# Kernel tuning notes

Hardware: AMD Instinct MI355X
Metric: run time of the kernel (lower is better)

The kernel has to match this reference:

```python
import jax, jax.numpy as jnp
import numpy as np

V, D, H, HD, T, FF, L = 32000, 1024, 16, 64, 1024, 4096, 8
B, S = 2, 1024
EPS = 1e-5


def setup_inputs() -> dict:
    key = jax.random.key(0)
    ks = jax.random.split(key, 14)
    s = 0.02
    return {
        "input_ids": jax.random.randint(ks[0], (B, S), 0, V),
        "emb": jax.random.normal(ks[1], (V, D), jnp.float32) * s,
        "Wu": jax.random.normal(ks[2], (L, 3 * T, D), jnp.float32) * s,
        "Wo": jax.random.normal(ks[3], (L, D, T), jnp.float32) * s,
        "n1w": jnp.ones((L, D), jnp.float32),
        "n1b": jnp.zeros((L, D), jnp.float32),
        "n2w": jnp.ones((L, D), jnp.float32),
        "n2b": jnp.zeros((L, D), jnp.float32),
        "f1w": jax.random.normal(ks[4], (L, FF, D), jnp.float32) * s,
        "f1b": jnp.zeros((L, FF), jnp.float32),
        "f2w": jax.random.normal(ks[5], (L, D, FF), jnp.float32) * s,
        "f2b": jnp.zeros((L, D), jnp.float32),
        "fnw": jnp.ones((D,), jnp.float32),
        "fnb": jnp.zeros((D,), jnp.float32),
    }


def _layernorm(x, w, b):
    mu = jnp.mean(x, -1, keepdims=True)
    var = jnp.mean((x - mu) ** 2, -1, keepdims=True)
    return (x - mu) * jax.lax.rsqrt(var + EPS) * w + b


def _rope_tables(seq_len, dtype):
    inv_freq = 1.0 / (10000.0 ** (jnp.arange(0, HD, 2, dtype=jnp.float32) / HD))
    freqs = jnp.arange(seq_len, dtype=jnp.float32)[:, None] * inv_freq[None, :]
    emb = jnp.concatenate([freqs, freqs], -1)  # [S, HD]
    return jnp.cos(emb).astype(dtype), jnp.sin(emb).astype(dtype)


def _rotate_half(x):
    x1, x2 = x[..., : HD // 2], x[..., HD // 2 :]
    return jnp.concatenate([-x2, x1], -1)


def _attn(x, Wu, Wo):
    b, s, _ = x.shape
    u = jnp.einsum("bsd,ed->bse", x, Wu)  # [B,S,3T]
    def split_heads(t):
        return t.reshape(b, s, H, HD).transpose(0, 2, 1, 3)  # [B,H,S,HD]
    q = split_heads(u[..., :T])
    k = split_heads(u[..., T : 2 * T])
    v = split_heads(u[..., 2 * T :])
    cos, sin = _rope_tables(s, x.dtype)  # [S,HD] -> broadcast [1,1,S,HD]
    cos, sin = cos[None, None], sin[None, None]
    q = q * cos + _rotate_half(q) * sin
    k = k * cos + _rotate_half(k) * sin
    scores = jnp.einsum("bhqd,bhkd->bhqk", q, k) / jnp.sqrt(jnp.asarray(HD, x.dtype))
    causal = jnp.tril(jnp.ones((s, s), bool))
    scores = jnp.where(causal[None, None], scores, jnp.asarray(-jnp.inf, x.dtype))
    probs = jax.nn.softmax(scores, -1)
    out = jnp.einsum("bhqk,bhkd->bhqd", probs, v)
    out = out.transpose(0, 2, 1, 3).reshape(b, s, T)
    return jnp.einsum("bst,dt->bsd", out, Wo)


def reference(input_ids, emb, Wu, Wo, n1w, n1b, n2w, n2b, f1w, f1b, f2w, f2b, fnw, fnb):
    x = emb[input_ids]  # [B,S,D]
    for i in range(L):
        x = x + _attn(_layernorm(x, n1w[i], n1b[i]), Wu[i], Wo[i])
        h = _layernorm(x, n2w[i], n2b[i])
        h = jax.nn.gelu(jnp.einsum("bsd,fd->bsf", h, f1w[i]) + f1b[i], approximate=False)
        x = x + jnp.einsum("bsf,df->bsd", h, f2w[i]) + f2b[i]
    x = _layernorm(x, fnw, fnb)
    return jnp.einsum("bsd,vd->bsv", x, emb)  # tied output head
```

## Files before the change

kernel.cpp:

```cpp
#include <hip/hip_runtime.h>

typedef unsigned short u16;
typedef unsigned int u32;
typedef __bf16 bf16x8 __attribute__((ext_vector_type(8)));
typedef float f32x4 __attribute__((ext_vector_type(4)));

static constexpr int S_ = 1024, D_ = 1024, H_ = 16, T_ = 1024, FF_ = 4096, L_ = 8, V_ = 32000, B_ = 2;
static constexpr int M_ = B_ * S_;

#define DEV static __device__ __forceinline__

DEV u16 f2bf(float f){ u32 u = __float_as_uint(f); u += 0x7fffu + ((u >> 16) & 1u); return (u16)(u >> 16); }
DEV float bf2f(u16 h){ return __uint_as_float(((u32)h) << 16); }

__global__ __launch_bounds__(256) void k_cvt(const float* __restrict__ src, u16* __restrict__ dst, long n4){
  long i = (long)blockIdx.x * 256 + threadIdx.x;
  if (i >= n4) return;
  float4 v = ((const float4*)src)[i];
  ushort4 o; o.x = f2bf(v.x); o.y = f2bf(v.y); o.z = f2bf(v.z); o.w = f2bf(v.w);
  ((ushort4*)dst)[i] = o;
}

__global__ __launch_bounds__(256) void k_embed(const int* __restrict__ ids, const float* __restrict__ emb, float* __restrict__ x){
  int m = blockIdx.x;
  int id = ids[m];
  float4 v = ((const float4*)(emb + (size_t)id * D_))[threadIdx.x];
  ((float4*)(x + (size_t)m * D_))[threadIdx.x] = v;
}

__global__ __launch_bounds__(256) void k_ln(const float* __restrict__ x, const float* __restrict__ w,
                                            const float* __restrict__ b, u16* __restrict__ out){
  int row = blockIdx.x, t = threadIdx.x;
  float4 v = ((const float4*)(x + (size_t)row * D_))[t];
  float s = v.x + v.y + v.z + v.w;
  for (int off = 32; off; off >>= 1) s += __shfl_xor(s, off, 64);
  __shared__ float red[8];
  int wid = t >> 6, lane = t & 63;
  if (!lane) red[wid] = s;
  __syncthreads();
  float mu = (red[0] + red[1] + red[2] + red[3]) * (1.f / D_);
  float dx = v.x - mu, dy = v.y - mu, dz = v.z - mu, dw = v.w - mu;
  float s2 = dx*dx + dy*dy + dz*dz + dw*dw;
  for (int off = 32; off; off >>= 1) s2 += __shfl_xor(s2, off, 64);
  if (!lane) red[4 + wid] = s2;
  __syncthreads();
  float rs = rsqrtf((red[4] + red[5] + red[6] + red[7]) * (1.f / D_) + 1e-5f);
  float4 wv = ((const float4*)w)[t], bv = ((const float4*)b)[t];
  ushort4 o;
  o.x = f2bf(dx * rs * wv.x + bv.x);
  o.y = f2bf(dy * rs * wv.y + bv.y);
  o.z = f2bf(dz * rs * wv.z + bv.z);
  o.w = f2bf(dw * rs * wv.w + bv.w);
  ((ushort4*)(out + (size_t)row * D_))[t] = o;
}

__global__ __launch_bounds__(256) void k_rope(const float* __restrict__ u, u16* __restrict__ qb,
                                              u16* __restrict__ kb, u16* __restrict__ vb){
  int m = blockIdx.x;
  int b = m >> 10, s = m & (S_ - 1);
  const float* ur = u + (size_t)m * (3 * T_);
  for (int i = threadIdx.x; i < T_; i += 256){
    int h = i >> 6, d = i & 63, d2 = d & 31;
    float inv = expf(-(float)d2 * 0.28782313662425572f);
    float ang = (float)s * inv;
    float c, sn; sincosf(ang, &sn, &c);
    float qa = ur[i],      ka = ur[T_ + i];
    float qp = ur[i ^ 32], kp = ur[T_ + (i ^ 32)];
    float sgn = (d & 32) ? 1.f : -1.f;
    size_t o = ((size_t)(b * H_ + h) * S_ + s) * 64 + d;
    qb[o] = f2bf(qa * c + sgn * qp * sn);
    kb[o] = f2bf(ka * c + sgn * kp * sn);
    vb[o] = f2bf(ur[2 * T_ + i]);
  }
}

__global__ __launch_bounds__(256) void k_attn(const u16* __restrict__ qb, const u16* __restrict__ kb,
                                              const u16* __restrict__ vb, u16* __restrict__ out){
  __shared__ float qt[16][68];
  __shared__ float kt[64][65];
  __shared__ float vt[64][64];
  __shared__ float pr[16][64];
  int q0 = blockIdx.x * 16;
  int bh = blockIdx.y;
  int b = bh >> 4, hh = bh & 15;
  const u16* qp = qb + (size_t)bh * S_ * 64;
  const u16* kp = kb + (size_t)bh * S_ * 64;
  const u16* vp = vb + (size_t)bh * S_ * 64;
  int t = threadIdx.x;
  for (int i = t; i < 16 * 64; i += 256){
    int r = i >> 6, d = i & 63;
    qt[r][d] = bf2f(qp[(size_t)(q0 + r) * 64 + d]) * 0.125f;
  }
  int row = t >> 4, l16 = t & 15;
  int qrow = q0 + row;
  float m_i = -1e30f, l_i = 0.f;
  float o0 = 0.f, o1 = 0.f, o2 = 0.f, o3 = 0.f;
  int ktmax = q0 >> 6;
  __syncthreads();
  for (int kti = 0; kti <= ktmax; ++kti){
    int k0 = kti << 6;
    for (int i = t; i < 64 * 64; i += 256){
      int r = i >> 6, d = i & 63;
      kt[r][d] = bf2f(kp[(size_t)(k0 + r) * 64 + d]);
      vt[r][d] = bf2f(vp[(size_t)(k0 + r) * 64 + d]);
    }
    __syncthreads();
    float sc[4];
    for (int jj = 0; jj < 4; ++jj){
      int ks = l16 * 4 + jj;
      float a = 0.f;
      for (int d = 0; d < 64; ++d) a += qt[row][d] * kt[ks][d];
      sc[jj] = (k0 + ks <= qrow) ? a : -1e30f;
    }
    float tm = fmaxf(fmaxf(sc[0], sc[1]), fmaxf(sc[2], sc[3]));
    for (int off = 8; off; off >>= 1) tm = fmaxf(tm, __shfl_xor(tm, off, 16));
    float nm = fmaxf(m_i, tm);
    float al = expf(m_i - nm);
    float p0 = expf(sc[0] - nm), p1 = expf(sc[1] - nm), p2 = expf(sc[2] - nm), p3 = expf(sc[3] - nm);
    float ps = p0 + p1 + p2 + p3;
    for (int off = 8; off; off >>= 1) ps += __shfl_xor(ps, off, 16);
    l_i = l_i * al + ps; m_i = nm;
    o0 *= al; o1 *= al; o2 *= al; o3 *= al;
    float4 pv4; pv4.x = p0; pv4.y = p1; pv4.z = p2; pv4.w = p3;
    *(float4*)&pr[row][l16 * 4] = pv4;
    __syncthreads();
    for (int k = 0; k < 64; ++k){
      float pk = pr[row][k];
      float4 vv = *(const float4*)&vt[k][l16 * 4];
      o0 += pk * vv.x; o1 += pk * vv.y; o2 += pk * vv.z; o3 += pk * vv.w;
    }
    __syncthreads();
  }
  float il = 1.f / l_i;
  ushort4 ov; ov.x = f2bf(o0 * il); ov.y = f2bf(o1 * il); ov.z = f2bf(o2 * il); ov.w = f2bf(o3 * il);
  *(ushort4*)&out[(size_t)(b * S_ + qrow) * T_ + hh * 64 + l16 * 4] = ov;
}

__global__ __launch_bounds__(256) void k_gemm(const u16* __restrict__ A, const u16* __restrict__ B,
                                              int M, int N, int K,
                                              float* C, const float* __restrict__ bias,
                                              const float* res, u16* Cbf, int epi){
  __shared__ __align__(16) u16 la[128 * 40];
  __shared__ __align__(16) u16 lb[128 * 40];
  int t = threadIdx.x;
  int wave = t >> 6, lane = t & 63;
  int wm = (wave >> 1) << 6, wn = (wave & 1) << 6;
  int quad = lane >> 4, l16 = lane & 15;
  long mB = (long)blockIdx.y << 7;
  long nB = (long)blockIdx.x << 7;
  int sr  = t >> 2;
  int sc8 = (t & 3) << 3;
  f32x4 acc[4][4];
  for (int i = 0; i < 4; ++i)
    for (int j = 0; j < 4; ++j)
      for (int r = 0; r < 4; ++r) acc[i][j][r] = 0.f;
  const u16* Ap0 = A + (mB + sr) * (long)K + sc8;
  const u16* Bp0 = B + (nB + sr) * (long)K + sc8;
  for (int k0 = 0; k0 < K; k0 += 32){
    uint4 a0 = *(const uint4*)(Ap0 + k0);
    uint4 a1 = *(const uint4*)(Ap0 + (long)64 * K + k0);
    uint4 b0 = *(const uint4*)(Bp0 + k0);
    uint4 b1 = *(const uint4*)(Bp0 + (long)64 * K + k0);
    *(uint4*)&la[sr * 40 + sc8] = a0;
    *(uint4*)&la[(sr + 64) * 40 + sc8] = a1;
    *(uint4*)&lb[sr * 40 + sc8] = b0;
    *(uint4*)&lb[(sr + 64) * 40 + sc8] = b1;
    __syncthreads();
    bf16x8 af[4], bfv[4];
    for (int i = 0; i < 4; ++i) af[i]  = *(const bf16x8*)&la[(wm + i * 16 + l16) * 40 + quad * 8];
    for (int j = 0; j < 4; ++j) bfv[j] = *(const bf16x8*)&lb[(wn + j * 16 + l16) * 40 + quad * 8];
    for (int i = 0; i < 4; ++i)
      for (int j = 0; j < 4; ++j)
        acc[i][j] = __builtin_amdgcn_mfma_f32_16x16x32_bf16(af[i], bfv[j], acc[i][j], 0, 0, 0);
    __syncthreads();
  }
  for (int i = 0; i < 4; ++i){
    int gr = (int)mB + wm + i * 16 + quad * 4;
    for (int j = 0; j < 4; ++j){
      int gc = (int)nB + wn + j * 16 + l16;
      float bval = (bias && epi != 0) ? bias[gc] : 0.f;
      for (int r = 0; r < 4; ++r){
        long idx = (long)(gr + r) * N + gc;
        float v = acc[i][j][r];
        if (epi == 0){ C[idx] = v; }
        else if (epi == 1){ v += bval; Cbf[idx] = f2bf(0.5f * v * (1.f + erff(v * 0.70710678118f))); }
        else { v += res[idx] + bval; C[idx] = v; }
      }
    }
  }
}

extern "C" void kernel_launch(void* const* d_in, const int* in_sizes, int n_in,
                              void* d_out, int out_size, void* d_ws, size_t ws_size,
                              hipStream_t stream){
  const int*   ids = (const int*)  d_in[0];
  const float* emb = (const float*)d_in[1];
  const float* Wu  = (const float*)d_in[2];
  const float* Wo  = (const float*)d_in[3];
  const float* n1w = (const float*)d_in[4];
  const float* n1b = (const float*)d_in[5];
  const float* n2w = (const float*)d_in[6];
  const float* n2b = (const float*)d_in[7];
  const float* f1w = (const float*)d_in[8];
  const float* f1b = (const float*)d_in[9];
  const float* f2w = (const float*)d_in[10];
  const float* f2b = (const float*)d_in[11];
  const float* fnw = (const float*)d_in[12];
  const float* fnb = (const float*)d_in[13];

  char* p = (char*)d_ws;
  auto alloc = [&](size_t bytes) -> void* { void* r = p; p += (bytes + 255) & ~(size_t)255; return r; };
  u16*   wEmb = (u16*)  alloc((size_t)V_ * D_ * 2);
  u16*   wWuL = (u16*)  alloc((size_t)3 * T_ * D_ * 2);
  u16*   wWoL = (u16*)  alloc((size_t)D_ * T_ * 2);
  u16*   wF1L = (u16*)  alloc((size_t)FF_ * D_ * 2);
  u16*   wF2L = (u16*)  alloc((size_t)D_ * FF_ * 2);
  float* x    = (float*)alloc((size_t)M_ * D_ * 4);
  float* u    = (float*)alloc((size_t)M_ * 3 * T_ * 4);
  u16*   actbf= (u16*)  alloc((size_t)M_ * D_ * 2);
  u16*   qb   = (u16*)  alloc((size_t)M_ * T_ * 2);
  u16*   kb   = (u16*)  alloc((size_t)M_ * T_ * 2);
  u16*   vb   = (u16*)  alloc((size_t)M_ * T_ * 2);
  u16*   h    = (u16*)u;

  auto cvt = [&](const float* s, u16* d, long n){
    long n4 = n / 4;
    k_cvt<<<dim3((unsigned)((n4 + 255) / 256)), 256, 0, stream>>>(s, d, n4);
  };

  k_embed<<<M_, 256, 0, stream>>>(ids, emb, x);

  for (int i = 0; i < L_; ++i){
    cvt(Wu  + (size_t)i * 3 * T_ * D_, wWuL, (long)3 * T_ * D_);
    cvt(Wo  + (size_t)i * D_ * T_,     wWoL, (long)D_ * T_);
    cvt(f1w + (size_t)i * FF_ * D_,    wF1L, (long)FF_ * D_);
    cvt(f2w + (size_t)i * D_ * FF_,    wF2L, (long)D_ * FF_);

    k_ln<<<M_, 256, 0, stream>>>(x, n1w + i * D_, n1b + i * D_, actbf);
    k_gemm<<<dim3(3 * T_ / 128, M_ / 128), 256, 0, stream>>>(actbf, wWuL, M_, 3 * T_, D_,
                                                             u, nullptr, nullptr, nullptr, 0);
    k_rope<<<M_, 256, 0, stream>>>(u, qb, kb, vb);
    k_attn<<<dim3(S_ / 16, B_ * H_), 256, 0, stream>>>(qb, kb, vb, actbf);
    k_gemm<<<dim3(D_ / 128, M_ / 128), 256, 0, stream>>>(actbf, wWoL, M_, D_, T_,
                                                         x, nullptr, x, nullptr, 2);
    k_ln<<<M_, 256, 0, stream>>>(x, n2w + i * D_, n2b + i * D_, actbf);
    k_gemm<<<dim3(FF_ / 128, M_ / 128), 256, 0, stream>>>(actbf, wF1L, M_, FF_, D_,
                                                          nullptr, f1b + (size_t)i * FF_, nullptr, h, 1);
    k_gemm<<<dim3(D_ / 128, M_ / 128), 256, 0, stream>>>(h, wF2L, M_, D_, FF_,
                                                         x, f2b + (size_t)i * D_, x, nullptr, 2);
  }

  cvt(emb, wEmb, (long)V_ * D_);
  k_ln<<<M_, 256, 0, stream>>>(x, fnw, fnb, actbf);
  k_gemm<<<dim3(V_ / 128, M_ / 128), 256, 0, stream>>>(actbf, wEmb, M_, V_, D_,
                                                       (float*)d_out, nullptr, nullptr, nullptr, 0);
}
```

Before: 10.79 ms.

## Register-prefetch GEMM tiles, swap grid order, and restructure attention inner loops

The GEMM now loads the next K-slice of A and B into registers while the MFMAs run on the current shared-memory tile. This is meant to hide global load latency, at the cost of more live registers. The launch grid is also swapped so consecutive blocks walk along M for the same weight N-tile, which should improve L2 reuse of weight tiles. Attention keeps Q in registers, uses vectorized K/V staging, lays out scores with a stride-16 key mapping, and drops one barrier per key tile. This last change relies on warp-level ordering for the pr buffer, which risks a race.

```diff
diff --git a/kernel.cpp b/kernel.cpp
--- a/kernel.cpp
+++ b/kernel.cpp
@@ -76,10 +76,9 @@
 
 __global__ __launch_bounds__(256) void k_attn(const u16* __restrict__ qb, const u16* __restrict__ kb,
                                               const u16* __restrict__ vb, u16* __restrict__ out){
-  __shared__ float qt[16][68];
-  __shared__ float kt[64][65];
+  __shared__ float kt[64][68];
   __shared__ float vt[64][64];
-  __shared__ float pr[16][64];
+  __shared__ float pr[16][68];
   int q0 = blockIdx.x * 16;
   int bh = blockIdx.y;
   int b = bh >> 4, hh = bh & 15;
@@ -87,49 +86,73 @@
   const u16* kp = kb + (size_t)bh * S_ * 64;
   const u16* vp = vb + (size_t)bh * S_ * 64;
   int t = threadIdx.x;
-  for (int i = t; i < 16 * 64; i += 256){
-    int r = i >> 6, d = i & 63;
-    qt[r][d] = bf2f(qp[(size_t)(q0 + r) * 64 + d]) * 0.125f;
-  }
   int row = t >> 4, l16 = t & 15;
   int qrow = q0 + row;
+  float4 qv[16];
+  const ushort4* qr = (const ushort4*)(qp + (size_t)qrow * 64);
+  #pragma unroll
+  for (int d4 = 0; d4 < 16; ++d4){
+    ushort4 u4 = qr[d4];
+    qv[d4].x = bf2f(u4.x) * 0.125f;
+    qv[d4].y = bf2f(u4.y) * 0.125f;
+    qv[d4].z = bf2f(u4.z) * 0.125f;
+    qv[d4].w = bf2f(u4.w) * 0.125f;
+  }
   float m_i = -1e30f, l_i = 0.f;
   float o0 = 0.f, o1 = 0.f, o2 = 0.f, o3 = 0.f;
   int ktmax = q0 >> 6;
-  __syncthreads();
   for (int kti = 0; kti <= ktmax; ++kti){
     int k0 = kti << 6;
-    for (int i = t; i < 64 * 64; i += 256){
-      int r = i >> 6, d = i & 63;
-      kt[r][d] = bf2f(kp[(size_t)(k0 + r) * 64 + d]);
-      vt[r][d] = bf2f(vp[(size_t)(k0 + r) * 64 + d]);
-    }
-    __syncthreads();
-    float sc[4];
-    for (int jj = 0; jj < 4; ++jj){
-      int ks = l16 * 4 + jj;
-      float a = 0.f;
-      for (int d = 0; d < 64; ++d) a += qt[row][d] * kt[ks][d];
-      sc[jj] = (k0 + ks <= qrow) ? a : -1e30f;
-    }
-    float tm = fmaxf(fmaxf(sc[0], sc[1]), fmaxf(sc[2], sc[3]));
+    __syncthreads();
+    for (int i = t; i < 64 * 16; i += 256){
+      int r = i >> 4, d4 = i & 15;
+      ushort4 kv = ((const ushort4*)(kp + (size_t)(k0 + r) * 64))[d4];
+      ushort4 vv = ((const ushort4*)(vp + (size_t)(k0 + r) * 64))[d4];
+      float4 kf, vf;
+      kf.x = bf2f(kv.x); kf.y = bf2f(kv.y); kf.z = bf2f(kv.z); kf.w = bf2f(kv.w);
+      vf.x = bf2f(vv.x); vf.y = bf2f(vv.y); vf.z = bf2f(vv.z); vf.w = bf2f(vv.w);
+      *(float4*)&kt[r][d4 * 4] = kf;
+      *(float4*)&vt[r][d4 * 4] = vf;
+    }
+    __syncthreads();
+    float sc0 = 0.f, sc1 = 0.f, sc2 = 0.f, sc3 = 0.f;
+    #pragma unroll
+    for (int d4 = 0; d4 < 16; ++d4){
+      float4 q4 = qv[d4];
+      float4 ka = *(const float4*)&kt[l16][d4 * 4];
+      float4 kb4 = *(const float4*)&kt[16 + l16][d4 * 4];
+      float4 kc = *(const float4*)&kt[32 + l16][d4 * 4];
+      float4 kd = *(const float4*)&kt[48 + l16][d4 * 4];
+      sc0 += q4.x*ka.x + q4.y*ka.y + q4.z*ka.z + q4.w*ka.w;
+      sc1 += q4.x*kb4.x + q4.y*kb4.y + q4.z*kb4.z + q4.w*kb4.w;
+      sc2 += q4.x*kc.x + q4.y*kc.y + q4.z*kc.z + q4.w*kc.w;
+      sc3 += q4.x*kd.x + q4.y*kd.y + q4.z*kd.z + q4.w*kd.w;
+    }
+    sc0 = (k0 + l16      <= qrow) ? sc0 : -1e30f;
+    sc1 = (k0 + 16 + l16 <= qrow) ? sc1 : -1e30f;
+    sc2 = (k0 + 32 + l16 <= qrow) ? sc2 : -1e30f;
+    sc3 = (k0 + 48 + l16 <= qrow) ? sc3 : -1e30f;
+    float tm = fmaxf(fmaxf(sc0, sc1), fmaxf(sc2, sc3));
     for (int off = 8; off; off >>= 1) tm = fmaxf(tm, __shfl_xor(tm, off, 16));
     float nm = fmaxf(m_i, tm);
     float al = expf(m_i - nm);
-    float p0 = expf(sc[0] - nm), p1 = expf(sc[1] - nm), p2 = expf(sc[2] - nm), p3 = expf(sc[3] - nm);
+    float p0 = expf(sc0 - nm), p1 = expf(sc1 - nm), p2 = expf(sc2 - nm), p3 = expf(sc3 - nm);
     float ps = p0 + p1 + p2 + p3;
     for (int off = 8; off; off >>= 1) ps += __shfl_xor(ps, off, 16);
     l_i = l_i * al + ps; m_i = nm;
     o0 *= al; o1 *= al; o2 *= al; o3 *= al;
-    float4 pv4; pv4.x = p0; pv4.y = p1; pv4.z = p2; pv4.w = p3;
-    *(float4*)&pr[row][l16 * 4] = pv4;
-    __syncthreads();
-    for (int k = 0; k < 64; ++k){
-      float pk = pr[row][k];
-      float4 vv = *(const float4*)&vt[k][l16 * 4];
-      o0 += pk * vv.x; o1 += pk * vv.y; o2 += pk * vv.z; o3 += pk * vv.w;
-    }
-    __syncthreads();
+    pr[row][l16]      = p0;
+    pr[row][16 + l16] = p1;
+    pr[row][32 + l16] = p2;
+    pr[row][48 + l16] = p3;
+    #pragma unroll
+    for (int k4 = 0; k4 < 16; ++k4){
+      float4 p4 = *(const float4*)&pr[row][k4 * 4];
+      { float4 vv = *(const float4*)&vt[k4 * 4 + 0][l16 * 4]; o0 += p4.x*vv.x; o1 += p4.x*vv.y; o2 += p4.x*vv.z; o3 += p4.x*vv.w; }
+      { float4 vv = *(const float4*)&vt[k4 * 4 + 1][l16 * 4]; o0 += p4.y*vv.x; o1 += p4.y*vv.y; o2 += p4.y*vv.z; o3 += p4.y*vv.w; }
+      { float4 vv = *(const float4*)&vt[k4 * 4 + 2][l16 * 4]; o0 += p4.z*vv.x; o1 += p4.z*vv.y; o2 += p4.z*vv.z; o3 += p4.z*vv.w; }
+      { float4 vv = *(const float4*)&vt[k4 * 4 + 3][l16 * 4]; o0 += p4.w*vv.x; o1 += p4.w*vv.y; o2 += p4.w*vv.z; o3 += p4.w*vv.w; }
+    }
   }
   float il = 1.f / l_i;
   ushort4 ov; ov.x = f2bf(o0 * il); ov.y = f2bf(o1 * il); ov.z = f2bf(o2 * il); ov.w = f2bf(o3 * il);
@@ -146,8 +169,8 @@
   int wave = t >> 6, lane = t & 63;
   int wm = (wave >> 1) << 6, wn = (wave & 1) << 6;
   int quad = lane >> 4, l16 = lane & 15;
-  long mB = (long)blockIdx.y << 7;
-  long nB = (long)blockIdx.x << 7;
+  long mB = (long)blockIdx.x << 7;
+  long nB = (long)blockIdx.y << 7;
   int sr  = t >> 2;
   int sc8 = (t & 3) << 3;
   f32x4 acc[4][4];
@@ -156,16 +179,22 @@
       for (int r = 0; r < 4; ++r) acc[i][j][r] = 0.f;
   const u16* Ap0 = A + (mB + sr) * (long)K + sc8;
   const u16* Bp0 = B + (nB + sr) * (long)K + sc8;
+  uint4 a0 = *(const uint4*)(Ap0);
+  uint4 a1 = *(const uint4*)(Ap0 + (long)64 * K);
+  uint4 b0 = *(const uint4*)(Bp0);
+  uint4 b1 = *(const uint4*)(Bp0 + (long)64 * K);
   for (int k0 = 0; k0 < K; k0 += 32){
-    uint4 a0 = *(const uint4*)(Ap0 + k0);
-    uint4 a1 = *(const uint4*)(Ap0 + (long)64 * K + k0);
-    uint4 b0 = *(const uint4*)(Bp0 + k0);
-    uint4 b1 = *(const uint4*)(Bp0 + (long)64 * K + k0);
     *(uint4*)&la[sr * 40 + sc8] = a0;
     *(uint4*)&la[(sr + 64) * 40 + sc8] = a1;
     *(uint4*)&lb[sr * 40 + sc8] = b0;
     *(uint4*)&lb[(sr + 64) * 40 + sc8] = b1;
     __syncthreads();
+    if (k0 + 32 < K){
+      a0 = *(const uint4*)(Ap0 + k0 + 32);
+      a1 = *(const uint4*)(Ap0 + (long)64 * K + k0 + 32);
+      b0 = *(const uint4*)(Bp0 + k0 + 32);
+      b1 = *(const uint4*)(Bp0 + (long)64 * K + k0 + 32);
+    }
     bf16x8 af[4], bfv[4];
     for (int i = 0; i < 4; ++i) af[i]  = *(const bf16x8*)&la[(wm + i * 16 + l16) * 40 + quad * 8];
     for (int j = 0; j < 4; ++j) bfv[j] = *(const bf16x8*)&lb[(wn + j * 16 + l16) * 40 + quad * 8];
@@ -237,21 +266,21 @@
     cvt(f2w + (size_t)i * D_ * FF_,    wF2L, (long)D_ * FF_);
 
     k_ln<<<M_, 256, 0, stream>>>(x, n1w + i * D_, n1b + i * D_, actbf);
-    k_gemm<<<dim3(3 * T_ / 128, M_ / 128), 256, 0, stream>>>(actbf, wWuL, M_, 3 * T_, D_,
+    k_gemm<<<dim3(M_ / 128, 3 * T_ / 128), 256, 0, stream>>>(actbf, wWuL, M_, 3 * T_, D_,
                                                              u, nullptr, nullptr, nullptr, 0);
     k_rope<<<M_, 256, 0, stream>>>(u, qb, kb, vb);
     k_attn<<<dim3(S_ / 16, B_ * H_), 256, 0, stream>>>(qb, kb, vb, actbf);
-    k_gemm<<<dim3(D_ / 128, M_ / 128), 256, 0, stream>>>(actbf, wWoL, M_, D_, T_,
+    k_gemm<<<dim3(M_ / 128, D_ / 128), 256, 0, stream>>>(actbf, wWoL, M_, D_, T_,
                                                          x, nullptr, x, nullptr, 2);
     k_ln<<<M_, 256, 0, stream>>>(x, n2w + i * D_, n2b + i * D_, actbf);
-    k_gemm<<<dim3(FF_ / 128, M_ / 128), 256, 0, stream>>>(actbf, wF1L, M_, FF_, D_,
+    k_gemm<<<dim3(M_ / 128, FF_ / 128), 256, 0, stream>>>(actbf, wF1L, M_, FF_, D_,
                                                           nullptr, f1b + (size_t)i * FF_, nullptr, h, 1);
-    k_gemm<<<dim3(D_ / 128, M_ / 128), 256, 0, stream>>>(h, wF2L, M_, D_, FF_,
+    k_gemm<<<dim3(M_ / 128, D_ / 128), 256, 0, stream>>>(h, wF2L, M_, D_, FF_,
                                                          x, f2b + (size_t)i * D_, x, nullptr, 2);
   }
 
   cvt(emb, wEmb, (long)V_ * D_);
   k_ln<<<M_, 256, 0, stream>>>(x, fnw, fnb, actbf);
-  k_gemm<<<dim3(V_ / 128, M_ / 128), 256, 0, stream>>>(actbf, wEmb, M_, V_, D_,
+  k_gemm<<<dim3(M_ / 128, V_ / 128), 256, 0, stream>>>(actbf, wEmb, M_, V_, D_,
                                                        (float*)d_out, nullptr, nullptr, nullptr, 0);
 }
```

Measured after the change: 9.293 ms. -13.9%, faster.
